# Optimization experiments

Measured on AMD Instinct MI355X. Metric: run time of the kernel, lower is better.

Reference implementation:

```python
import jax, jax.numpy as jnp
import numpy as np

NB_FEATURES = 256
DIM_HEADS = 64
CHUNK = 128  # chunk length for the causal prefix-sum scan (exact, chunking-invariant)
KERNEL_EPS = 1e-6


def _gaussian_orthogonal(nb_rows, nb_cols, seed=0):
    # Mirrors gaussian_orthogonal_random_matrix with scaling=0.
    rng = np.random.default_rng(seed)
    blocks = []
    n_full = nb_rows // nb_cols
    for _ in range(n_full):
        q, _ = np.linalg.qr(rng.standard_normal((nb_cols, nb_cols)))
        blocks.append(q.T)
    rem = nb_rows - n_full * nb_cols
    if rem > 0:
        q, _ = np.linalg.qr(rng.standard_normal((nb_cols, nb_cols)))
        blocks.append(q.T[:rem])
    mat = np.concatenate(blocks, 0)
    multiplier = np.linalg.norm(rng.standard_normal((nb_rows, nb_cols)), axis=1)
    return (multiplier[:, None] * mat).astype(np.float32)


def setup_inputs() -> dict:
    key = jax.random.key(0)
    kq, kk, kv = jax.random.split(key, 3)
    shape = (2, 8, 4096, DIM_HEADS)  # [b, h, n, d]
    return {
        "q": jax.random.normal(kq, shape, dtype=jnp.float32),
        "k": jax.random.normal(kk, shape, dtype=jnp.float32),
        "v": jax.random.normal(kv, shape, dtype=jnp.float32),
        "proj": jnp.asarray(_gaussian_orthogonal(NB_FEATURES, DIM_HEADS)),
    }


def _generalized_kernel(x, proj):
    # generalized_kernel with kernel_fn=sigmoid, normalize_data=True
    normalizer = x.shape[-1] ** (-0.25)
    scores = jnp.einsum('bhnd,md->bhnm', normalizer * x, proj)
    return jax.nn.sigmoid(scores) + KERNEL_EPS


def _causal_linear_attention(qp, kp, v):
    # Exact causal linear attention: out_n = q'_n . (sum_{m<=n} k'_m v_m^T) / (q'_n . (cumsum k')_n + eps-term)
    b, h, n, m = qp.shape
    e = v.shape[-1]
    nc = n // CHUNK

    def split(t):
        return jnp.moveaxis(t.reshape(b, h, nc, CHUNK, t.shape[-1]), 2, 0)

    qs, ks, vs = split(qp), split(kp), split(v)

    def step(carry, xs):
        k_last, S_last = carry              # [b,h,m], [b,h,m,e]
        qc, kc, vc = xs                     # [b,h,c,m], [b,h,c,m], [b,h,c,e]
        k_cum = k_last[:, :, None, :] + jnp.cumsum(kc, axis=2)
        D_inv = 1.0 / jnp.einsum('bhcm,bhcm->bhc', qc, k_cum + KERNEL_EPS)
        ctx = jnp.einsum('bhcm,bhce->bhcme', kc, vc)          # per-position outer products
        S_cum = S_last[:, :, None] + jnp.cumsum(ctx, axis=2)  # running state [b,h,c,m,e]
        out = jnp.einsum('bhcme,bhcm,bhc->bhce', S_cum, qc, D_inv)
        return (k_cum[:, :, -1], S_cum[:, :, -1]), out

    init = (jnp.zeros((b, h, m), qp.dtype), jnp.zeros((b, h, m, e), qp.dtype))
    _, outs = jax.lax.scan(step, init, (qs, ks, vs))          # [nc,b,h,c,e]
    return jnp.moveaxis(outs, 0, 2).reshape(b, h, n, e)


def reference(q, k, v, proj):
    qp = _generalized_kernel(q, proj)
    kp = _generalized_kernel(k, proj)
    return _causal_linear_attention(qp, kp, v)
```

## Files before the change

### kernel.cpp

```cpp
#include <hip/hip_runtime.h>
#include <hip/hip_bf16.h>

#define NORM 0.35355339059327373f
#define EPS 1e-6f

typedef __attribute__((ext_vector_type(8))) short short8;
typedef __attribute__((ext_vector_type(4))) float floatx4;

static __device__ __forceinline__ ushort f2bf(float x) {
  union { __hip_bfloat16 h; ushort u; } c;
  c.h = __float2bfloat16(x);
  return c.u;
}
static __device__ __forceinline__ ushort2 f2bf2(float a, float b) {
  union { __hip_bfloat162 h; ushort2 u; } c;
  c.h = __float22bfloat162_rn(make_float2(a, b));
  return c.u;
}
static __device__ __forceinline__ float sigm(float s) {
  return __builtin_amdgcn_rcpf(1.f + __expf(-s)) + EPS;
}
#define MFMA __builtin_amdgcn_mfma_f32_16x16x32_bf16


__global__ __launch_bounds__(256) void k0_proj(const float* __restrict__ proj,
                                               ushort* __restrict__ prjg) {
  int id = blockIdx.x * 256 + threadIdx.x;
  float4 a = ((const float4*)proj)[id];
  ushort2 lo = f2bf2(a.x * NORM, a.y * NORM);
  ushort2 hi = f2bf2(a.z * NORM, a.w * NORM);
  ((ushort4*)prjg)[id] = make_ushort4(lo.x, lo.y, hi.x, hi.y);
}

__global__ __launch_bounds__(512, 4) void k1_chunksums(
    const float* __restrict__ k, const float* __restrict__ v,
    const ushort* __restrict__ prjg, float* __restrict__ ksumg,
    ushort* __restrict__ stg) {
  __shared__ __align__(16) ushort xk[128 * 72];
  __shared__ __align__(16) ushort vt[80 * 136];
  __shared__ __align__(16) ushort kpt[64 * 136];
  const int t = threadIdx.x;
  const int w = t >> 6, l = t & 63, lr = l & 15, lg = l >> 4;
  const int blk = blockIdx.x;
  const float4* kg4 = (const float4*)(k + (size_t)blk * 8192);
  const float4* vg4 = (const float4*)(v + (size_t)blk * 8192);

  #pragma unroll
  for (int u = 0; u < 4; ++u) {
    int id = t + u * 512;
    float4 a = kg4[id];
    int row = id >> 4, c = (id & 15) * 4;
    ushort2 p0 = f2bf2(a.x, a.y), p1 = f2bf2(a.z, a.w);
    *(ushort4*)&xk[row * 72 + c] = make_ushort4(p0.x, p0.y, p1.x, p1.y);
  }
  #pragma unroll
  for (int u = 0; u < 4; ++u) {
    int id = t + u * 512;
    float4 a = vg4[id];
    int pos = id >> 4, e = (id & 15) * 4;
    vt[(e + 0) * 136 + pos] = f2bf(a.x);
    vt[(e + 1) * 136 + pos] = f2bf(a.y);
    vt[(e + 2) * 136 + pos] = f2bf(a.z);
    vt[(e + 3) * 136 + pos] = f2bf(a.w);
  }
  #pragma unroll
  for (int u = 0; u < 4; ++u) {
    int id = t + u * 512;
    int rr = id >> 7, pos = id & 127;
    vt[(64 + rr) * 136 + pos] = (rr == 0) ? (ushort)0x3F80 : (ushort)0;
  }
  __syncthreads();

  const int fb = w & 3, g = w >> 2;
  float* kb = ksumg + (size_t)blk * 256;
  ushort* stbp = stg + (size_t)blk * 16384;

  for (int qd = 0; qd < 4; ++qd) {
    {
      short8 a0 = *(const short8*)&xk[(w * 16 + lr) * 72 + lg * 8];
      short8 a1 = *(const short8*)&xk[(w * 16 + lr) * 72 + 32 + lg * 8];
      #pragma unroll
      for (int fb2 = 0; fb2 < 4; ++fb2) {
        short8 b0 = *(const short8*)&prjg[(size_t)(qd * 64 + fb2 * 16 + lr) * 64 + lg * 8];
        short8 b1 = *(const short8*)&prjg[(size_t)(qd * 64 + fb2 * 16 + lr) * 64 + 32 + lg * 8];
        floatx4 fa = (floatx4){0.f, 0.f, 0.f, 0.f};
        fa = MFMA(a0, b0, fa, 0, 0, 0);
        fa = MFMA(a1, b1, fa, 0, 0, 0);
        ushort2 p0 = f2bf2(sigm(fa[0]), sigm(fa[1]));
        ushort2 p1 = f2bf2(sigm(fa[2]), sigm(fa[3]));
        *(ushort4*)&kpt[(fb2 * 16 + lr) * 136 + w * 16 + lg * 4] =
            make_ushort4(p0.x, p0.y, p1.x, p1.y);
      }
    }
    __syncthreads();

    {
      floatx4 s0 = (floatx4){0.f, 0.f, 0.f, 0.f};
      floatx4 s1 = (floatx4){0.f, 0.f, 0.f, 0.f};
      floatx4 s2 = (floatx4){0.f, 0.f, 0.f, 0.f};
      #pragma unroll
      for (int ks = 0; ks < 4; ++ks) {
        short8 a = *(const short8*)&kpt[(fb * 16 + lr) * 136 + ks * 32 + lg * 8];
        short8 bA = *(const short8*)&vt[(g * 16 + lr) * 136 + ks * 32 + lg * 8];
        s0 = MFMA(a, bA, s0, 0, 0, 0);
        short8 bB = *(const short8*)&vt[((2 + g) * 16 + lr) * 136 + ks * 32 + lg * 8];
        s1 = MFMA(a, bB, s1, 0, 0, 0);
        if (g == 0) {
          short8 bC = *(const short8*)&vt[(64 + lr) * 136 + ks * 32 + lg * 8];
          s2 = MFMA(a, bC, s2, 0, 0, 0);
        }
      }
      {
        ushort2 q0 = f2bf2(s0[0], s0[1]), q1 = f2bf2(s0[2], s0[3]);
        *(ushort4*)&stbp[(size_t)(g * 16 + lr) * 256 + qd * 64 + fb * 16 + lg * 4] =
            make_ushort4(q0.x, q0.y, q1.x, q1.y);
        ushort2 r0_ = f2bf2(s1[0], s1[1]), r1_ = f2bf2(s1[2], s1[3]);
        *(ushort4*)&stbp[(size_t)((2 + g) * 16 + lr) * 256 + qd * 64 + fb * 16 + lg * 4] =
            make_ushort4(r0_.x, r0_.y, r1_.x, r1_.y);
      }
      if (g == 0 && lr == 0) {
        #pragma unroll
        for (int r = 0; r < 4; ++r) kb[qd * 64 + fb * 16 + lg * 4 + r] = s2[r];
      }
    }
    __syncthreads();
  }
}

__global__ __launch_bounds__(256) void k2_scan(float* __restrict__ ksumg,
                                               ushort* __restrict__ stg) {
  int bh = blockIdx.x / 33, part = blockIdx.x % 33, t = threadIdx.x;
  if (part < 32) {
    int e2 = part * 256 + t;
    uint* p = (uint*)stg + (size_t)bh * 32 * 8192 + e2;
    float r0 = 0.f, r1 = 0.f;
    #pragma unroll 4
    for (int c = 0; c < 32; ++c) {
      uint u = p[(size_t)c * 8192];
      float a = __uint_as_float(u << 16);
      float b = __uint_as_float(u & 0xffff0000u);
      ushort2 w2 = f2bf2(r0, r1);
      p[(size_t)c * 8192] = (uint)w2.x | ((uint)w2.y << 16);
      r0 += a; r1 += b;
    }
  } else {
    float run = 0.f;
    float* p = ksumg + (size_t)bh * 32 * 256 + t;
    #pragma unroll 4
    for (int c = 0; c < 32; ++c) {
      float tmp = p[(size_t)c * 256];
      p[(size_t)c * 256] = run;
      run += tmp;
    }
  }
}

__global__ __launch_bounds__(512, 4) void k3_out(
    const float* __restrict__ q, const float* __restrict__ k,
    const float* __restrict__ v, const ushort* __restrict__ prjg,
    const float* __restrict__ ksumg, const ushort* __restrict__ stg,
    float* __restrict__ out) {
  __shared__ __align__(16) union U0 {
    struct { ushort xq[128 * 72]; ushort xk[128 * 72]; } s;
    ushort ab[128 * 136];
  } r0;
  __shared__ __align__(16) union U1 {
    ushort qp[128 * 72];
    ushort vt[64 * 136];
  } r1;
  __shared__ __align__(16) ushort kp[144 * 72];
  __shared__ float den[128];

  const int t = threadIdx.x;
  const int w = t >> 6, l = t & 63, lr = l & 15, lg = l >> 4;
  const int blk = blockIdx.x;
  const float4* qg4 = (const float4*)(q + (size_t)blk * 8192);
  const float4* kg4 = (const float4*)(k + (size_t)blk * 8192);
  const float4* vg4 = (const float4*)(v + (size_t)blk * 8192);
  const float* ksb = ksumg + (size_t)blk * 256;
  const ushort* stb = stg + (size_t)blk * 16384;
  float* outg = out + (size_t)blk * 8192;

  float kv0 = 0.f, kv1 = 0.f, kv2 = 0.f, kv3 = 0.f;
  if (t < 64) {
    kv0 = ksb[t]; kv1 = ksb[64 + t]; kv2 = ksb[128 + t]; kv3 = ksb[192 + t];
  }
  for (int id = t; id < 1080; id += 512) kp[9288 + id] = (ushort)0;

  #pragma unroll
  for (int u = 0; u < 4; ++u) {
    int id = t + u * 512;
    float4 a = qg4[id];
    float4 c = kg4[id];
    int row = id >> 4, cc = (id & 15) * 4;
    ushort2 a0 = f2bf2(a.x, a.y), a1 = f2bf2(a.z, a.w);
    *(ushort4*)&r0.s.xq[row * 72 + cc] = make_ushort4(a0.x, a0.y, a1.x, a1.y);
    ushort2 c0 = f2bf2(c.x, c.y), c1 = f2bf2(c.z, c.w);
    *(ushort4*)&r0.s.xk[row * 72 + cc] = make_ushort4(c0.x, c0.y, c1.x, c1.y);
  }
  __syncthreads();

  floatx4 Aacc[9];
  floatx4 Oacc[4];
  #pragma unroll
  for (int i = 0; i < 9; ++i) Aacc[i] = (floatx4){0.f, 0.f, 0.f, 0.f};
  #pragma unroll
  for (int i = 0; i < 4; ++i) Oacc[i] = (floatx4){0.f, 0.f, 0.f, 0.f};
  const int px = w & 1, fbw = w >> 1;
  const int eb = w & 3, qh = w >> 2;

  for (int qd = 0; qd < 4; ++qd) {
    short8 pj0 = *(const short8*)&prjg[(size_t)(qd * 64 + fbw * 16 + lr) * 64 + lg * 8];
    short8 pj1 = *(const short8*)&prjg[(size_t)(qd * 64 + fbw * 16 + lr) * 64 + 32 + lg * 8];
    short8 st0 = *(const short8*)&stb[(size_t)(eb * 16 + lr) * 256 + qd * 64 + lg * 8];
    short8 st1 = *(const short8*)&stb[(size_t)(eb * 16 + lr) * 256 + qd * 64 + 32 + lg * 8];
    if (t < 64) {
      float kvq = qd == 0 ? kv0 : qd == 1 ? kv1 : qd == 2 ? kv2 : kv3;
      kp[9216 + t] = f2bf(kvq + EPS);
    }
    const ushort* xb = px ? r0.s.xk : r0.s.xq;
    ushort* xp = px ? kp : r1.qp;
    #pragma unroll
    for (int h = 0; h < 2; ++h) {
      floatx4 fa[4];
      #pragma unroll
      for (int i = 0; i < 4; ++i) fa[i] = (floatx4){0.f, 0.f, 0.f, 0.f};
      #pragma unroll
      for (int ks2 = 0; ks2 < 2; ++ks2) {
        short8 a = ks2 ? pj1 : pj0;
        #pragma unroll
        for (int nb4 = 0; nb4 < 4; ++nb4) {
          int nb = h * 4 + nb4;
          short8 b = *(const short8*)&xb[(nb * 16 + lr) * 72 + ks2 * 32 + lg * 8];
          fa[nb4] = MFMA(a, b, fa[nb4], 0, 0, 0);
        }
      }
      #pragma unroll
      for (int nb4 = 0; nb4 < 4; ++nb4) {
        int nb = h * 4 + nb4;
        ushort2 p0 = f2bf2(sigm(fa[nb4][0]), sigm(fa[nb4][1]));
        ushort2 p1 = f2bf2(sigm(fa[nb4][2]), sigm(fa[nb4][3]));
        *(ushort4*)&xp[(nb * 16 + lr) * 72 + fbw * 16 + lg * 4] =
            make_ushort4(p0.x, p0.y, p1.x, p1.y);
      }
    }
    __syncthreads();

    #pragma unroll
    for (int ks = 0; ks < 2; ++ks) {
      short8 aq = *(const short8*)&r1.qp[(w * 16 + lr) * 72 + ks * 32 + lg * 8];
      #pragma unroll
      for (int nb = 0; nb < 8; ++nb) {
        if (nb <= w) {
          short8 bk = *(const short8*)&kp[(nb * 16 + lr) * 72 + ks * 32 + lg * 8];
          Aacc[nb] = MFMA(aq, bk, Aacc[nb], 0, 0, 0);
        }
      }
      short8 bx = *(const short8*)&kp[(128 + lr) * 72 + ks * 32 + lg * 8];
      Aacc[8] = MFMA(aq, bx, Aacc[8], 0, 0, 0);
    }
    #pragma unroll
    for (int ks = 0; ks < 2; ++ks) {
      short8 as = ks ? st1 : st0;
      #pragma unroll
      for (int nq = 0; nq < 4; ++nq) {
        int jb = qh * 4 + nq;
        short8 bq = *(const short8*)&r1.qp[(jb * 16 + lr) * 72 + ks * 32 + lg * 8];
        Oacc[nq] = MFMA(as, bq, Oacc[nq], 0, 0, 0);
      }
    }
    __syncthreads();
  }

  float4 fva = vg4[t], fvb = vg4[t + 512], fvc = vg4[t + 1024], fvd = vg4[t + 1536];

  #pragma unroll
  for (int r = 0; r < 4; ++r) {
    const int qrow = w * 16 + lg * 4 + r;
    float s = 0.f;
    #pragma unroll
    for (int nb = 0; nb < 8; ++nb) {
      float val = Aacc[nb][r];
      if (nb * 16 + lr > qrow) val = 0.f;
      Aacc[nb][r] = val;
      s += val;
    }
    s += __shfl_xor(s, 1); s += __shfl_xor(s, 2);
    s += __shfl_xor(s, 4); s += __shfl_xor(s, 8);
    if (lr == 0) den[qrow] = s + Aacc[8][r];
  }
  #pragma unroll
  for (int nb = 0; nb < 8; ++nb) {
    #pragma unroll
    for (int r = 0; r < 4; ++r) {
      r0.ab[(w * 16 + lg * 4 + r) * 136 + nb * 16 + lr] = f2bf(Aacc[nb][r]);
    }
  }
  #pragma unroll
  for (int u = 0; u < 4; ++u) {
    float4 a = (u == 0) ? fva : (u == 1) ? fvb : (u == 2) ? fvc : fvd;
    int id = t + u * 512;
    int pos = id >> 4, e = (id & 15) * 4;
    r1.vt[(e + 0) * 136 + pos] = f2bf(a.x);
    r1.vt[(e + 1) * 136 + pos] = f2bf(a.y);
    r1.vt[(e + 2) * 136 + pos] = f2bf(a.z);
    r1.vt[(e + 3) * 136 + pos] = f2bf(a.w);
  }
  __syncthreads();

  #pragma unroll
  for (int ks = 0; ks < 4; ++ks) {
    short8 av = *(const short8*)&r1.vt[(eb * 16 + lr) * 136 + ks * 32 + lg * 8];
    #pragma unroll
    for (int nq = 0; nq < 4; ++nq) {
      int jb = qh * 4 + nq;
      if (ks <= (jb >> 1)) {
        short8 ba = *(const short8*)&r0.ab[(jb * 16 + lr) * 136 + ks * 32 + lg * 8];
        Oacc[nq] = MFMA(av, ba, Oacc[nq], 0, 0, 0);
      }
    }
  }
  #pragma unroll
  for (int nq = 0; nq < 4; ++nq) {
    const int qrow = (qh * 4 + nq) * 16 + lr;
    float dinv = __builtin_amdgcn_rcpf(den[qrow]);
    float4 o = make_float4(Oacc[nq][0] * dinv, Oacc[nq][1] * dinv,
                           Oacc[nq][2] * dinv, Oacc[nq][3] * dinv);
    *(float4*)(outg + (size_t)qrow * 64 + eb * 16 + lg * 4) = o;
  }
}

extern "C" void kernel_launch(void* const* d_in, const int* in_sizes, int n_in,
                              void* d_out, int out_size, void* d_ws, size_t ws_size,
                              hipStream_t stream) {
  const float* q = (const float*)d_in[0];
  const float* k = (const float*)d_in[1];
  const float* v = (const float*)d_in[2];
  const float* proj = (const float*)d_in[3];
  float* out = (float*)d_out;
  ushort* prjg = (ushort*)d_ws;
  float* ksumg = (float*)((char*)d_ws + 32768);
  ushort* stg = (ushort*)((char*)d_ws + 32768 + 524288);

  k0_proj<<<16, 256, 0, stream>>>(proj, prjg);
  k1_chunksums<<<512, 512, 0, stream>>>(k, v, prjg, ksumg, stg);
  k2_scan<<<16 * 33, 256, 0, stream>>>(ksumg, stg);
  k3_out<<<512, 512, 0, stream>>>(q, k, v, prjg, ksumg, stg, out);
}
```

Baseline: 69.80 us.

## Double-buffer k1 feature tile, prefetch proj/state in k3, add MFMA priority

k1 double-buffers its per-quarter feature tile in shared memory, which lets it drop the trailing barrier of each loop iteration. k3 prefetches the next quarter's projection and state fragments into registers, and issues the V loads one iteration early. s_setprio is raised around the MFMA sections, and the scan unroll goes from 4 to 8. The aim is to hide global load latency and shorten barrier stalls, at the cost of more LDS in k1 and more registers in k3, which could lower occupancy.

```diff
diff --git a/kernel.cpp b/kernel.cpp
--- a/kernel.cpp
+++ b/kernel.cpp
@@ -38,7 +38,7 @@
     ushort* __restrict__ stg) {
   __shared__ __align__(16) ushort xk[128 * 72];
   __shared__ __align__(16) ushort vt[80 * 136];
-  __shared__ __align__(16) ushort kpt[64 * 136];
+  __shared__ __align__(16) ushort kpt[2 * 64 * 136];
   const int t = threadIdx.x;
   const int w = t >> 6, l = t & 63, lr = l & 15, lg = l >> 4;
   const int blk = blockIdx.x;
@@ -76,6 +76,7 @@
   ushort* stbp = stg + (size_t)blk * 16384;
 
   for (int qd = 0; qd < 4; ++qd) {
+    ushort* kq = kpt + (qd & 1) * 8704;
     {
       short8 a0 = *(const short8*)&xk[(w * 16 + lr) * 72 + lg * 8];
       short8 a1 = *(const short8*)&xk[(w * 16 + lr) * 72 + 32 + lg * 8];
@@ -88,7 +89,7 @@
         fa = MFMA(a1, b1, fa, 0, 0, 0);
         ushort2 p0 = f2bf2(sigm(fa[0]), sigm(fa[1]));
         ushort2 p1 = f2bf2(sigm(fa[2]), sigm(fa[3]));
-        *(ushort4*)&kpt[(fb2 * 16 + lr) * 136 + w * 16 + lg * 4] =
+        *(ushort4*)&kq[(fb2 * 16 + lr) * 136 + w * 16 + lg * 4] =
             make_ushort4(p0.x, p0.y, p1.x, p1.y);
       }
     }
@@ -98,9 +99,10 @@
       floatx4 s0 = (floatx4){0.f, 0.f, 0.f, 0.f};
       floatx4 s1 = (floatx4){0.f, 0.f, 0.f, 0.f};
       floatx4 s2 = (floatx4){0.f, 0.f, 0.f, 0.f};
+      __builtin_amdgcn_s_setprio(1);
       #pragma unroll
       for (int ks = 0; ks < 4; ++ks) {
-        short8 a = *(const short8*)&kpt[(fb * 16 + lr) * 136 + ks * 32 + lg * 8];
+        short8 a = *(const short8*)&kq[(fb * 16 + lr) * 136 + ks * 32 + lg * 8];
         short8 bA = *(const short8*)&vt[(g * 16 + lr) * 136 + ks * 32 + lg * 8];
         s0 = MFMA(a, bA, s0, 0, 0, 0);
         short8 bB = *(const short8*)&vt[((2 + g) * 16 + lr) * 136 + ks * 32 + lg * 8];
@@ -110,6 +112,7 @@
           s2 = MFMA(a, bC, s2, 0, 0, 0);
         }
       }
+      __builtin_amdgcn_s_setprio(0);
       {
         ushort2 q0 = f2bf2(s0[0], s0[1]), q1 = f2bf2(s0[2], s0[3]);
         *(ushort4*)&stbp[(size_t)(g * 16 + lr) * 256 + qd * 64 + fb * 16 + lg * 4] =
@@ -123,7 +126,6 @@
         for (int r = 0; r < 4; ++r) kb[qd * 64 + fb * 16 + lg * 4 + r] = s2[r];
       }
     }
-    __syncthreads();
   }
 }
 
@@ -134,7 +136,7 @@
     int e2 = part * 256 + t;
     uint* p = (uint*)stg + (size_t)bh * 32 * 8192 + e2;
     float r0 = 0.f, r1 = 0.f;
-    #pragma unroll 4
+    #pragma unroll 8
     for (int c = 0; c < 32; ++c) {
       uint u = p[(size_t)c * 8192];
       float a = __uint_as_float(u << 16);
@@ -146,7 +148,7 @@
   } else {
     float run = 0.f;
     float* p = ksumg + (size_t)bh * 32 * 256 + t;
-    #pragma unroll 4
+    #pragma unroll 8
     for (int c = 0; c < 32; ++c) {
       float tmp = p[(size_t)c * 256];
       p[(size_t)c * 256] = run;
@@ -208,12 +210,17 @@
   for (int i = 0; i < 4; ++i) Oacc[i] = (floatx4){0.f, 0.f, 0.f, 0.f};
   const int px = w & 1, fbw = w >> 1;
   const int eb = w & 3, qh = w >> 2;
-
+  float4 fva, fvb, fvc, fvd;
+
+  short8 pjc[2][2], stc[2][2];
+  pjc[0][0] = *(const short8*)&prjg[(size_t)(fbw * 16 + lr) * 64 + lg * 8];
+  pjc[0][1] = *(const short8*)&prjg[(size_t)(fbw * 16 + lr) * 64 + 32 + lg * 8];
+  stc[0][0] = *(const short8*)&stb[(size_t)(eb * 16 + lr) * 256 + lg * 8];
+  stc[0][1] = *(const short8*)&stb[(size_t)(eb * 16 + lr) * 256 + 32 + lg * 8];
+
+  #pragma unroll
   for (int qd = 0; qd < 4; ++qd) {
-    short8 pj0 = *(const short8*)&prjg[(size_t)(qd * 64 + fbw * 16 + lr) * 64 + lg * 8];
-    short8 pj1 = *(const short8*)&prjg[(size_t)(qd * 64 + fbw * 16 + lr) * 64 + 32 + lg * 8];
-    short8 st0 = *(const short8*)&stb[(size_t)(eb * 16 + lr) * 256 + qd * 64 + lg * 8];
-    short8 st1 = *(const short8*)&stb[(size_t)(eb * 16 + lr) * 256 + qd * 64 + 32 + lg * 8];
+    const int cur = qd & 1, nxt = cur ^ 1;
     if (t < 64) {
       float kvq = qd == 0 ? kv0 : qd == 1 ? kv1 : qd == 2 ? kv2 : kv3;
       kp[9216 + t] = f2bf(kvq + EPS);
@@ -227,7 +234,7 @@
       for (int i = 0; i < 4; ++i) fa[i] = (floatx4){0.f, 0.f, 0.f, 0.f};
       #pragma unroll
       for (int ks2 = 0; ks2 < 2; ++ks2) {
-        short8 a = ks2 ? pj1 : pj0;
+        short8 a = pjc[cur][ks2];
         #pragma unroll
         for (int nb4 = 0; nb4 < 4; ++nb4) {
           int nb = h * 4 + nb4;
@@ -246,6 +253,17 @@
     }
     __syncthreads();
 
+    if (qd < 3) {
+      pjc[nxt][0] = *(const short8*)&prjg[(size_t)((qd + 1) * 64 + fbw * 16 + lr) * 64 + lg * 8];
+      pjc[nxt][1] = *(const short8*)&prjg[(size_t)((qd + 1) * 64 + fbw * 16 + lr) * 64 + 32 + lg * 8];
+      stc[nxt][0] = *(const short8*)&stb[(size_t)(eb * 16 + lr) * 256 + (qd + 1) * 64 + lg * 8];
+      stc[nxt][1] = *(const short8*)&stb[(size_t)(eb * 16 + lr) * 256 + (qd + 1) * 64 + 32 + lg * 8];
+    }
+    if (qd == 3) {
+      fva = vg4[t]; fvb = vg4[t + 512]; fvc = vg4[t + 1024]; fvd = vg4[t + 1536];
+    }
+
+    __builtin_amdgcn_s_setprio(1);
     #pragma unroll
     for (int ks = 0; ks < 2; ++ks) {
       short8 aq = *(const short8*)&r1.qp[(w * 16 + lr) * 72 + ks * 32 + lg * 8];
@@ -261,7 +279,7 @@
     }
     #pragma unroll
     for (int ks = 0; ks < 2; ++ks) {
-      short8 as = ks ? st1 : st0;
+      short8 as = stc[cur][ks];
       #pragma unroll
       for (int nq = 0; nq < 4; ++nq) {
         int jb = qh * 4 + nq;
@@ -269,10 +287,9 @@
         Oacc[nq] = MFMA(as, bq, Oacc[nq], 0, 0, 0);
       }
     }
+    __builtin_amdgcn_s_setprio(0);
     __syncthreads();
   }
-
-  float4 fva = vg4[t], fvb = vg4[t + 512], fvc = vg4[t + 1024], fvd = vg4[t + 1536];
 
   #pragma unroll
   for (int r = 0; r < 4; ++r) {
@@ -308,6 +325,7 @@
   }
   __syncthreads();
 
+  __builtin_amdgcn_s_setprio(1);
   #pragma unroll
   for (int ks = 0; ks < 4; ++ks) {
     short8 av = *(const short8*)&r1.vt[(eb * 16 + lr) * 136 + ks * 32 + lg * 8];
@@ -320,6 +338,7 @@
       }
     }
   }
+  __builtin_amdgcn_s_setprio(0);
   #pragma unroll
   for (int nq = 0; nq < 4; ++nq) {
     const int qrow = (qh * 4 + nq) * 16 + lr;
```

Result: faster. 66.75 us (-4.4%).
